# Kernel tuning notes

Measured on AMD Instinct MI355X. Metric: run time of the kernel, lower is better.

Reference implementation:

```python
import jax, jax.numpy as jnp
import numpy as np

N_SPK, N_UTT, D = 512, 64, 1024
EPS = 1e-6  # matches tf.math.l2_normalize default epsilon guard


def _l2norm(x, axis=-1):
    return x / jnp.sqrt(jnp.maximum(jnp.sum(x * x, axis=axis, keepdims=True), EPS))


def setup_inputs() -> dict:
    key = jax.random.key(0)
    k1, _ = jax.random.split(key)
    inputs = jax.random.normal(k1, (N_SPK, N_UTT, D), dtype=jnp.float32)
    w = jnp.asarray(10.0, dtype=jnp.float32)
    b = jnp.asarray(-5.0, dtype=jnp.float32)
    return {"inputs": inputs, "w": w, "b": b}


def reference(inputs, w, b):
    N, M, _ = inputs.shape
    # speaker centroids: mean over utterances -> [N, D]
    centroids = jnp.mean(inputs, axis=1)
    # utterance (exclusion) centroids: mean of the other M-1 utterances -> [N, M, D]
    ut_centroids = (jnp.sum(inputs, axis=1, keepdims=True) - inputs) / (M - 1)

    e = _l2norm(inputs)          # [N, M, D]
    c = _l2norm(centroids)       # [N, D]
    uc = _l2norm(ut_centroids)   # [N, M, D]

    # cosine sim of every utterance vs every speaker centroid -> [N, M, K]
    cos_all = jnp.einsum('nmd,kd->nmk', e, c)
    # same-speaker entries use the self-exclusion centroid
    cos_self = jnp.sum(e * uc, axis=-1)  # [N, M]
    eye = jnp.eye(N, dtype=inputs.dtype)[:, None, :]  # [N, 1, N]
    cos_sim = cos_all * (1.0 - eye) + cos_self[:, :, None] * eye

    sim = w * cos_sim + b  # [N, M, N]
    # softmax contrastive loss: -S_{j,i,j} + logsumexp_k S_{j,i,k}, summed
    lse = jax.nn.logsumexp(sim, axis=-1)            # [N, M]
    pos = jnp.einsum('nmn->nm', sim)                # diagonal along speaker axes
    loss = jnp.sum(lse - pos)
    return loss
```

## Files before the change

kernel.cpp:

```cpp
#include <hip/hip_runtime.h>
#include <stdint.h>

#define N_SPK 512
#define N_UTT 64
#define DIM   1024
#define NROWS (N_SPK * N_UTT)
#define EPS   1e-6f

#define BM  128
#define BN  128
#define BKB 128
#define KITERS (DIM / BKB)

typedef __attribute__((ext_vector_type(8))) int   int8v;
typedef __attribute__((ext_vector_type(4))) int   int4v;
typedef __attribute__((ext_vector_type(4))) float f32x4;

__global__ __launch_bounds__(256) void prep_stream(
    const float* __restrict__ x, uint8_t* __restrict__ xb,
    float* __restrict__ Sg4, float* __restrict__ xxg)
{
    const int b    = blockIdx.x;
    const int n    = b >> 2;
    const int g    = b & 3;
    const int tid  = threadIdx.x;
    const int lane = tid & 63;
    const int w    = tid >> 6;

    const float* xn  = x  + (size_t)n * N_UTT * DIM;
    uint8_t*     xbn = xb + (size_t)n * N_UTT * DIM;
    const int m0 = g * 16 + w * 4;

    float4 v[16];
    #pragma unroll
    for (int i = 0; i < 4; ++i)
        #pragma unroll
        for (int j = 0; j < 4; ++j)
            v[i * 4 + j] = *(const float4*)(xn + (size_t)(m0 + i) * DIM + j * 256 + lane * 4);

    float Sp[16];
    #pragma unroll
    for (int j = 0; j < 16; ++j) Sp[j] = 0.f;
    float xx[4] = {0.f, 0.f, 0.f, 0.f};

    #pragma unroll
    for (int i = 0; i < 4; ++i) {
        #pragma unroll
        for (int j = 0; j < 4; ++j) {
            const float4 q = v[i * 4 + j];
            xx[i] += q.x * q.x + q.y * q.y + q.z * q.z + q.w * q.w;
            Sp[j * 4 + 0] += q.x; Sp[j * 4 + 1] += q.y;
            Sp[j * 4 + 2] += q.z; Sp[j * 4 + 3] += q.w;
            uint32_t u = (uint32_t)__builtin_amdgcn_cvt_pk_fp8_f32(q.x, q.y, 0, false);
            u = (uint32_t)__builtin_amdgcn_cvt_pk_fp8_f32(q.z, q.w, (int)u, true);
            *(uint32_t*)(xbn + (size_t)(m0 + i) * DIM + j * 256 + lane * 4) = u;
        }
    }

    #pragma unroll
    for (int i = 0; i < 4; ++i) {
        float t = xx[i];
        #pragma unroll
        for (int off = 1; off < 64; off <<= 1) t += __shfl_xor(t, off);
        if (lane == 0) xxg[n * N_UTT + m0 + i] = t;
    }

    __shared__ float Sh[4][DIM];
    #pragma unroll
    for (int j = 0; j < 4; ++j)
        *(float4*)&Sh[w][j * 256 + lane * 4] =
            make_float4(Sp[j * 4], Sp[j * 4 + 1], Sp[j * 4 + 2], Sp[j * 4 + 3]);
    __syncthreads();

    const int d0 = tid * 4;
    float4 a = *(const float4*)&Sh[0][d0];
    const float4 b1 = *(const float4*)&Sh[1][d0];
    const float4 b2 = *(const float4*)&Sh[2][d0];
    const float4 b3 = *(const float4*)&Sh[3][d0];
    a.x += b1.x + b2.x + b3.x; a.y += b1.y + b2.y + b3.y;
    a.z += b1.z + b2.z + b3.z; a.w += b1.w + b2.w + b3.w;
    *(float4*)(Sg4 + ((size_t)g * N_SPK + n) * DIM + d0) = a;
}

__global__ __launch_bounds__(256) void centroid_kernel(
    const float* __restrict__ Sg4, uint8_t* __restrict__ cmat, float* __restrict__ ssqg)
{
    const int n   = blockIdx.x;
    const int tid = threadIdx.x;
    const int d0  = tid * 4;

    float4 S = *(const float4*)(Sg4 + (size_t)n * DIM + d0);
    #pragma unroll
    for (int g = 1; g < 4; ++g) {
        const float4 p = *(const float4*)(Sg4 + ((size_t)g * N_SPK + n) * DIM + d0);
        S.x += p.x; S.y += p.y; S.z += p.z; S.w += p.w;
    }

    float css = S.x * S.x + S.y * S.y + S.z * S.z + S.w * S.w;
    #pragma unroll
    for (int off = 1; off < 64; off <<= 1) css += __shfl_xor(css, off);
    __shared__ float red[4];
    if ((tid & 63) == 0) red[tid >> 6] = css;
    __syncthreads();
    const float ssq = red[0] + red[1] + red[2] + red[3];

    const float scale = rsqrtf(fmaxf(ssq * (1.0f / 4096.f), EPS)) * (16.0f / 64.f);
    uint32_t u = (uint32_t)__builtin_amdgcn_cvt_pk_fp8_f32(S.x * scale, S.y * scale, 0, false);
    u = (uint32_t)__builtin_amdgcn_cvt_pk_fp8_f32(S.z * scale, S.w * scale, (int)u, true);
    *(uint32_t*)(cmat + (size_t)n * DIM + d0) = u;
    if (tid == 0) ssqg[n] = ssq;
}

__global__ __launch_bounds__(256) void gemm_lse_kernel(
    const uint8_t* __restrict__ xb, const uint8_t* __restrict__ cmat,
    const float* __restrict__ xxg, const float* __restrict__ ssqg,
    const float* __restrict__ wp, const float* __restrict__ bp,
    float* __restrict__ sumexp4, float* __restrict__ pos)
{
    __shared__ __align__(16) uint8_t Asm[BM * BKB];
    __shared__ __align__(16) uint8_t Bsm[BN * BKB];
    __shared__ float SeLDS[BM];

    const int tid   = threadIdx.x;
    const int lane  = tid & 63;
    const int wid   = tid >> 6;
    const int waveM = wid >> 1;
    const int waveN = wid & 1;

    const int bid = blockIdx.x;
    const int rt  = (bid & 7) | ((bid >> 5) << 3);
    const int ct  = (bid >> 3) & 3;

    const int rowBase = rt * BM;
    const int colBase = ct * BN;

    const uint8_t* gA[4];
    const uint8_t* gB[4];
    #pragma unroll
    for (int i = 0; i < 4; ++i) {
        const int s    = i * 256 + tid;
        const int srow = s >> 3;
        const int h    = (s & 7) ^ (srow & 7);
        gA[i] = xb   + (size_t)(rowBase + srow) * DIM + h * 16;
        gB[i] = cmat + (size_t)(colBase + srow) * DIM + h * 16;
    }

    f32x4 acc[4][4];
    #pragma unroll
    for (int i = 0; i < 4; ++i)
        #pragma unroll
        for (int j = 0; j < 4; ++j)
            acc[i][j] = (f32x4){0.f, 0.f, 0.f, 0.f};

    const int cL  = lane & 15;
    const int q   = lane >> 4;
    const int fs0 = (2 * q) ^ (cL & 7);
    const int fs1 = fs0 ^ 1;

    for (int kt = 0; kt < KITERS; ++kt) {
        __syncthreads();
        const int ko = kt * BKB;
        #pragma unroll
        for (int i = 0; i < 4; ++i) {
            __builtin_amdgcn_global_load_lds(
                (const __attribute__((address_space(1))) void*)(gA[i] + ko),
                (__attribute__((address_space(3))) void*)(&Asm[(i * 256 + wid * 64) * 16]),
                16, 0, 0);
            __builtin_amdgcn_global_load_lds(
                (const __attribute__((address_space(1))) void*)(gB[i] + ko),
                (__attribute__((address_space(3))) void*)(&Bsm[(i * 256 + wid * 64) * 16]),
                16, 0, 0);
        }
        __syncthreads();

        int8v a[4], b[4];
        #pragma unroll
        for (int bi = 0; bi < 4; ++bi) {
            const int row = waveM * 64 + bi * 16 + cL;
            const int4v lo = *(const int4v*)&Asm[row * BKB + fs0 * 16];
            const int4v hi = *(const int4v*)&Asm[row * BKB + fs1 * 16];
            a[bi] = __builtin_shufflevector(lo, hi, 0, 1, 2, 3, 4, 5, 6, 7);
        }
        #pragma unroll
        for (int bj = 0; bj < 4; ++bj) {
            const int row = waveN * 64 + bj * 16 + cL;
            const int4v lo = *(const int4v*)&Bsm[row * BKB + fs0 * 16];
            const int4v hi = *(const int4v*)&Bsm[row * BKB + fs1 * 16];
            b[bj] = __builtin_shufflevector(lo, hi, 0, 1, 2, 3, 4, 5, 6, 7);
        }

        #pragma unroll
        for (int bi = 0; bi < 4; ++bi)
            #pragma unroll
            for (int bj = 0; bj < 4; ++bj)
                acc[bi][bj] = __builtin_amdgcn_mfma_scale_f32_16x16x128_f8f6f4(
                    a[bi], b[bj], acc[bi][bj],
                    0, 0,
                    0, 0x7f7f7f7f,
                    0, 0x7f7f7f7f);
    }

    const float wv = wp[0] * 0.0625f;
    const float bv = bp[0];
    float srow[16];
    #pragma unroll
    for (int bi = 0; bi < 4; ++bi) {
        #pragma unroll
        for (int r = 0; r < 4; ++r) {
            const int R     = rowBase + waveM * 64 + bi * 16 + q * 4 + r;
            const float xxv = xxg[R];
            const float rn  = rsqrtf(fmaxf(xxv, EPS));
            const int nrow  = R >> 6;
            float s = 0.f;
            #pragma unroll
            for (int bj = 0; bj < 4; ++bj) {
                const int col = colBase + waveN * 64 + bj * 16 + cL;
                const float dot = acc[bi][bj][r];
                float sim;
                if (col == nrow) {
                    const float ssqv = ssqg[nrow];
                    const float xs   = dot * sqrtf(ssqv) * 0.0625f;
                    const float d2   = ssqv - 2.f * xs + xxv;
                    const float cs   = ((xs - xxv) * (1.f / 63.f)) * rn *
                                       rsqrtf(fmaxf(d2 * (1.f / 3969.f), EPS));
                    sim = wp[0] * cs + bv;
                    pos[R] = sim;
                } else {
                    sim = wv * dot * rn + bv;
                }
                s += __expf(sim);
            }
            #pragma unroll
            for (int off = 1; off < 16; off <<= 1) s += __shfl_xor(s, off);
            srow[bi * 4 + r] = s;
        }
    }

    if (waveN == 1 && cL == 0) {
        #pragma unroll
        for (int bi = 0; bi < 4; ++bi)
            #pragma unroll
            for (int r = 0; r < 4; ++r)
                SeLDS[waveM * 64 + bi * 16 + q * 4 + r] = srow[bi * 4 + r];
    }
    __syncthreads();
    if (waveN == 0 && cL == 0) {
        #pragma unroll
        for (int bi = 0; bi < 4; ++bi)
            #pragma unroll
            for (int r = 0; r < 4; ++r) {
                const int lr = waveM * 64 + bi * 16 + q * 4 + r;
                sumexp4[(size_t)ct * NROWS + rowBase + lr] = srow[bi * 4 + r] + SeLDS[lr];
            }
    }
}

__global__ __launch_bounds__(1024) void finalize_kernel(
    const float* __restrict__ pos, const float* __restrict__ se4,
    float* __restrict__ out)
{
    const int tid = threadIdx.x;
    float acc = 0.f;
    for (int r = tid; r < NROWS; r += 1024) {
        const float s = se4[r] + se4[NROWS + r] + se4[2 * NROWS + r] + se4[3 * NROWS + r];
        acc += __logf(s) - pos[r];
    }
    #pragma unroll
    for (int off = 1; off < 64; off <<= 1) acc += __shfl_xor(acc, off);
    __shared__ float red[16];
    if ((tid & 63) == 0) red[tid >> 6] = acc;
    __syncthreads();
    if (tid == 0) {
        float t = 0.f;
        #pragma unroll
        for (int i = 0; i < 16; ++i) t += red[i];
        out[0] = t;
    }
}

extern "C" void kernel_launch(void* const* d_in, const int* in_sizes, int n_in,
                              void* d_out, int out_size, void* d_ws, size_t ws_size,
                              hipStream_t stream)
{
    const float* x  = (const float*)d_in[0];
    const float* wp = (const float*)d_in[1];
    const float* bp = (const float*)d_in[2];
    float* out = (float*)d_out;

    char* ws = (char*)d_ws;
    size_t off = 0;
    uint8_t*  xb      = (uint8_t*)(ws + off); off += (size_t)NROWS * DIM;
    uint8_t*  cmat    = (uint8_t*)(ws + off); off += (size_t)N_SPK * DIM;
    float*    Sg4     = (float*)(ws + off);   off += (size_t)4 * N_SPK * DIM * 4;
    float*    xxg     = (float*)(ws + off);   off += (size_t)NROWS * 4;
    float*    pos     = (float*)(ws + off);   off += (size_t)NROWS * 4;
    float*    sumexp4 = (float*)(ws + off);   off += (size_t)4 * NROWS * 4;
    float*    ssqg    = (float*)(ws + off);   off += (size_t)N_SPK * 4;

    prep_stream<<<N_SPK * 4, 256, 0, stream>>>(x, xb, Sg4, xxg);
    centroid_kernel<<<N_SPK, 256, 0, stream>>>(Sg4, cmat, ssqg);
    gemm_lse_kernel<<<(NROWS / BM) * (N_SPK / BN), 256, 0, stream>>>(
        xb, cmat, xxg, ssqg, wp, bp, sumexp4, pos);
    finalize_kernel<<<1, 1024, 0, stream>>>(pos, sumexp4, out);
}
```

Measured before the change: 278.8 us.

## Fuse centroid computation into prep kernel and cut GEMM register pressure

Merges prep_stream and centroid_kernel into one prep_full kernel. Each block now owns a whole speaker and loops over its 64 utterances, which removes the Sg4 partial-sum buffer, its global round trip and one launch. The GEMM kernel adds a min-blocks hint of 3 to launch_bounds and loads A fragments inside the bi loop rather than holding all four, to lower VGPR use and raise occupancy. The prep kernel now runs only 512 blocks and processes rows serially, so its memory-level parallelism drops.

```diff
diff --git a/kernel.cpp b/kernel.cpp
--- a/kernel.cpp
+++ b/kernel.cpp
@@ -16,53 +16,54 @@
 typedef __attribute__((ext_vector_type(4))) int   int4v;
 typedef __attribute__((ext_vector_type(4))) float f32x4;
 
-__global__ __launch_bounds__(256) void prep_stream(
+__global__ __launch_bounds__(256) void prep_full(
     const float* __restrict__ x, uint8_t* __restrict__ xb,
-    float* __restrict__ Sg4, float* __restrict__ xxg)
-{
-    const int b    = blockIdx.x;
-    const int n    = b >> 2;
-    const int g    = b & 3;
+    uint8_t* __restrict__ cmat, float* __restrict__ xxg, float* __restrict__ ssqg)
+{
+    const int n    = blockIdx.x;
     const int tid  = threadIdx.x;
     const int lane = tid & 63;
     const int w    = tid >> 6;
 
     const float* xn  = x  + (size_t)n * N_UTT * DIM;
     uint8_t*     xbn = xb + (size_t)n * N_UTT * DIM;
-    const int m0 = g * 16 + w * 4;
-
-    float4 v[16];
-    #pragma unroll
-    for (int i = 0; i < 4; ++i)
-        #pragma unroll
-        for (int j = 0; j < 4; ++j)
-            v[i * 4 + j] = *(const float4*)(xn + (size_t)(m0 + i) * DIM + j * 256 + lane * 4);
 
     float Sp[16];
     #pragma unroll
     for (int j = 0; j < 16; ++j) Sp[j] = 0.f;
-    float xx[4] = {0.f, 0.f, 0.f, 0.f};
-
-    #pragma unroll
-    for (int i = 0; i < 4; ++i) {
-        #pragma unroll
-        for (int j = 0; j < 4; ++j) {
-            const float4 q = v[i * 4 + j];
-            xx[i] += q.x * q.x + q.y * q.y + q.z * q.z + q.w * q.w;
-            Sp[j * 4 + 0] += q.x; Sp[j * 4 + 1] += q.y;
-            Sp[j * 4 + 2] += q.z; Sp[j * 4 + 3] += q.w;
-            uint32_t u = (uint32_t)__builtin_amdgcn_cvt_pk_fp8_f32(q.x, q.y, 0, false);
-            u = (uint32_t)__builtin_amdgcn_cvt_pk_fp8_f32(q.z, q.w, (int)u, true);
-            *(uint32_t*)(xbn + (size_t)(m0 + i) * DIM + j * 256 + lane * 4) = u;
-        }
-    }
-
-    #pragma unroll
-    for (int i = 0; i < 4; ++i) {
-        float t = xx[i];
-        #pragma unroll
-        for (int off = 1; off < 64; off <<= 1) t += __shfl_xor(t, off);
-        if (lane == 0) xxg[n * N_UTT + m0 + i] = t;
+
+    for (int rnd = 0; rnd < 4; ++rnd) {
+        const int m0 = w * 16 + rnd * 4;
+
+        float4 v[16];
+        #pragma unroll
+        for (int i = 0; i < 4; ++i)
+            #pragma unroll
+            for (int j = 0; j < 4; ++j)
+                v[i * 4 + j] = *(const float4*)(xn + (size_t)(m0 + i) * DIM + j * 256 + lane * 4);
+
+        float xx[4] = {0.f, 0.f, 0.f, 0.f};
+        #pragma unroll
+        for (int i = 0; i < 4; ++i) {
+            #pragma unroll
+            for (int j = 0; j < 4; ++j) {
+                const float4 q = v[i * 4 + j];
+                xx[i] += q.x * q.x + q.y * q.y + q.z * q.z + q.w * q.w;
+                Sp[j * 4 + 0] += q.x; Sp[j * 4 + 1] += q.y;
+                Sp[j * 4 + 2] += q.z; Sp[j * 4 + 3] += q.w;
+                uint32_t u = (uint32_t)__builtin_amdgcn_cvt_pk_fp8_f32(q.x, q.y, 0, false);
+                u = (uint32_t)__builtin_amdgcn_cvt_pk_fp8_f32(q.z, q.w, (int)u, true);
+                *(uint32_t*)(xbn + (size_t)(m0 + i) * DIM + j * 256 + lane * 4) = u;
+            }
+        }
+
+        #pragma unroll
+        for (int i = 0; i < 4; ++i) {
+            float t = xx[i];
+            #pragma unroll
+            for (int off = 1; off < 64; off <<= 1) t += __shfl_xor(t, off);
+            if (lane == 0) xxg[n * N_UTT + m0 + i] = t;
+        }
     }
 
     __shared__ float Sh[4][DIM];
@@ -73,27 +74,13 @@
     __syncthreads();
 
     const int d0 = tid * 4;
-    float4 a = *(const float4*)&Sh[0][d0];
-    const float4 b1 = *(const float4*)&Sh[1][d0];
-    const float4 b2 = *(const float4*)&Sh[2][d0];
-    const float4 b3 = *(const float4*)&Sh[3][d0];
-    a.x += b1.x + b2.x + b3.x; a.y += b1.y + b2.y + b3.y;
-    a.z += b1.z + b2.z + b3.z; a.w += b1.w + b2.w + b3.w;
-    *(float4*)(Sg4 + ((size_t)g * N_SPK + n) * DIM + d0) = a;
-}
-
-__global__ __launch_bounds__(256) void centroid_kernel(
-    const float* __restrict__ Sg4, uint8_t* __restrict__ cmat, float* __restrict__ ssqg)
-{
-    const int n   = blockIdx.x;
-    const int tid = threadIdx.x;
-    const int d0  = tid * 4;
-
-    float4 S = *(const float4*)(Sg4 + (size_t)n * DIM + d0);
-    #pragma unroll
-    for (int g = 1; g < 4; ++g) {
-        const float4 p = *(const float4*)(Sg4 + ((size_t)g * N_SPK + n) * DIM + d0);
-        S.x += p.x; S.y += p.y; S.z += p.z; S.w += p.w;
+    float4 S = *(const float4*)&Sh[0][d0];
+    {
+        const float4 b1 = *(const float4*)&Sh[1][d0];
+        const float4 b2 = *(const float4*)&Sh[2][d0];
+        const float4 b3 = *(const float4*)&Sh[3][d0];
+        S.x += b1.x + b2.x + b3.x; S.y += b1.y + b2.y + b3.y;
+        S.z += b1.z + b2.z + b3.z; S.w += b1.w + b2.w + b3.w;
     }
 
     float css = S.x * S.x + S.y * S.y + S.z * S.z + S.w * S.w;
@@ -111,7 +98,7 @@
     if (tid == 0) ssqg[n] = ssq;
 }
 
-__global__ __launch_bounds__(256) void gemm_lse_kernel(
+__global__ __launch_bounds__(256, 3) void gemm_lse_kernel(
     const uint8_t* __restrict__ xb, const uint8_t* __restrict__ cmat,
     const float* __restrict__ xxg, const float* __restrict__ ssqg,
     const float* __restrict__ wp, const float* __restrict__ bp,
@@ -173,14 +160,7 @@
         }
         __syncthreads();
 
-        int8v a[4], b[4];
-        #pragma unroll
-        for (int bi = 0; bi < 4; ++bi) {
-            const int row = waveM * 64 + bi * 16 + cL;
-            const int4v lo = *(const int4v*)&Asm[row * BKB + fs0 * 16];
-            const int4v hi = *(const int4v*)&Asm[row * BKB + fs1 * 16];
-            a[bi] = __builtin_shufflevector(lo, hi, 0, 1, 2, 3, 4, 5, 6, 7);
-        }
+        int8v b[4];
         #pragma unroll
         for (int bj = 0; bj < 4; ++bj) {
             const int row = waveN * 64 + bj * 16 + cL;
@@ -190,14 +170,19 @@
         }
 
         #pragma unroll
-        for (int bi = 0; bi < 4; ++bi)
+        for (int bi = 0; bi < 4; ++bi) {
+            const int row = waveM * 64 + bi * 16 + cL;
+            const int4v lo = *(const int4v*)&Asm[row * BKB + fs0 * 16];
+            const int4v hi = *(const int4v*)&Asm[row * BKB + fs1 * 16];
+            const int8v a = __builtin_shufflevector(lo, hi, 0, 1, 2, 3, 4, 5, 6, 7);
             #pragma unroll
             for (int bj = 0; bj < 4; ++bj)
                 acc[bi][bj] = __builtin_amdgcn_mfma_scale_f32_16x16x128_f8f6f4(
-                    a[bi], b[bj], acc[bi][bj],
+                    a, b[bj], acc[bi][bj],
                     0, 0,
                     0, 0x7f7f7f7f,
                     0, 0x7f7f7f7f);
+        }
     }
 
     const float wv = wp[0] * 0.0625f;
@@ -291,14 +276,12 @@
     size_t off = 0;
     uint8_t*  xb      = (uint8_t*)(ws + off); off += (size_t)NROWS * DIM;
     uint8_t*  cmat    = (uint8_t*)(ws + off); off += (size_t)N_SPK * DIM;
-    float*    Sg4     = (float*)(ws + off);   off += (size_t)4 * N_SPK * DIM * 4;
     float*    xxg     = (float*)(ws + off);   off += (size_t)NROWS * 4;
     float*    pos     = (float*)(ws + off);   off += (size_t)NROWS * 4;
     float*    sumexp4 = (float*)(ws + off);   off += (size_t)4 * NROWS * 4;
     float*    ssqg    = (float*)(ws + off);   off += (size_t)N_SPK * 4;
 
-    prep_stream<<<N_SPK * 4, 256, 0, stream>>>(x, xb, Sg4, xxg);
-    centroid_kernel<<<N_SPK, 256, 0, stream>>>(Sg4, cmat, ssqg);
+    prep_full<<<N_SPK, 256, 0, stream>>>(x, xb, cmat, xxg, ssqg);
     gemm_lse_kernel<<<(NROWS / BM) * (N_SPK / BN), 256, 0, stream>>>(
         xb, cmat, xxg, ssqg, wp, bp, sumexp4, pos);
     finalize_kernel<<<1, 1024, 0, stream>>>(pos, sumexp4, out);
```

New measurement: 561.3 us. 101% more time.
